# Optimization experiments

Hardware: AMD Instinct MI355X
Metric: run time of the kernel (lower is better)

The kernel has to match this reference:

```python
import jax, jax.numpy as jnp
import numpy as np

N, D, K = 20000, 128, 16   # nodes, distribution support size, padded neighbors (excl. self)
H = 2                      # number of barycenter hops (module's self.h)
EPS = 0.1                  # entropic regularization for the OT barycenter solver
SINK_ITERS = 20            # fixed Sinkhorn barycenter iterations
TINY = 1e-30


def setup_inputs() -> dict:
    key = jax.random.key(0)
    k1, k2, k3 = jax.random.split(key, 3)
    trans_X = jax.random.uniform(k1, (N, D), dtype=jnp.float32)
    costMatrix = jax.random.uniform(k2, (D, D), dtype=jnp.float32)
    neigh_idx = jax.random.randint(k3, (N, K), 0, N, dtype=jnp.int32)
    return {"trans_X": trans_X, "costMatrix": costMatrix, "neigh_idx": neigh_idx}


def _sinkhorn_barycenter(mu, Kmat, w):
    """Entropic Wasserstein barycenter (Benamou et al. iterative Bregman projections).
    mu:   [N, Kn, D] input distributions per node (rows sum to 1)
    Kmat: [D, D] Gibbs kernel exp(-C/eps)
    w:    [Kn] barycentric weights (sum to 1)
    returns b: [N, D] barycenter per node.
    """
    u0 = jnp.ones_like(mu)
    b0 = jnp.full(mu.shape[::2], 1.0 / mu.shape[-1], dtype=mu.dtype)  # [N, D]

    def step(carry, _):
        u, _b = carry
        # (K^T u): [N, Kn, D]
        KTu = jnp.einsum('ed,nke->nkd', Kmat, u) + TINY
        v = mu / KTu
        Kv = jnp.einsum('de,nke->nkd', Kmat, v) + TINY
        # geometric mean across the Kn input measures
        b = jnp.exp(jnp.einsum('k,nkd->nd', w, jnp.log(Kv)))
        u = b[:, None, :] / Kv
        return (u, b), None

    (_, b), _ = jax.lax.scan(step, (u0, b0), None, length=SINK_ITERS)
    return b


def reference(trans_X, costMatrix, neigh_idx):
    n = trans_X.shape[0]
    Kmat = jnp.exp(-costMatrix / EPS)  # [D, D]
    # append self node -> Kn = K + 1 members; uniform weights 1/degree (bary_weight='uniform')
    idx = jnp.concatenate([neigh_idx, jnp.arange(n, dtype=neigh_idx.dtype)[:, None]], axis=1)  # [N, Kn]
    Kn = idx.shape[1]
    w = jnp.full((Kn,), 1.0 / Kn, dtype=trans_X.dtype)

    X = trans_X
    for _ in range(H):
        mu = X[idx]                                    # gather neighbor dists [N, Kn, D]
        mu = mu / (jnp.sum(mu, axis=-1, keepdims=True) + TINY)
        X = _sinkhorn_barycenter(mu, Kmat, w)          # [N, D]
    return X
```

## Files before the change

### kernel.cpp

```cpp
#include <hip/hip_runtime.h>

#define D 128
#define NEIGH 16
#define SINKI 20
#define TINYF 1e-30f

typedef __attribute__((ext_vector_type(8))) _Float16 f16x8;
typedef __attribute__((ext_vector_type(2))) _Float16 f16x2;
typedef __attribute__((ext_vector_type(4))) float f32x4;
typedef __attribute__((ext_vector_type(2))) unsigned int u32x2;

template <int N>
__device__ __forceinline__ float rorf(float v) {
  int r = __builtin_amdgcn_update_dpp(0, __builtin_bit_cast(int, v),
                                      0x120 + N, 0xf, 0xf, true);
  return __builtin_bit_cast(float, r);
}

__device__ __forceinline__ f16x8 ldfrag(const _Float16* U, int k, int ks, int g) {
  return *(const f16x8*)((const char*)U + k * 256 + (((ks << 6) + (g << 4)) ^ ((k & 15) << 4)));
}

__device__ __forceinline__ void stquad(_Float16* U, int k, int rt, int g,
                                       float x, float y, float z, float w) {
  union { _Float16 h[4]; u32x2 u; } P;
  P.h[0] = (_Float16)x; P.h[1] = (_Float16)y;
  P.h[2] = (_Float16)z; P.h[3] = (_Float16)w;
  *(u32x2*)((char*)U + k * 256 + (((rt << 5) + (g << 3)) ^ ((k & 15) << 4))) = P.u;
}

__global__ __launch_bounds__(512, 1)
void wgcn_hop(const float* __restrict__ Xin,
              const float* __restrict__ Cmat,
              const int* __restrict__ neigh,
              float* __restrict__ Xout,
              int n_pairs) {
  __shared__ _Float16 KB[16384];
  __shared__ _Float16 KA[16384];
  __shared__ _Float16 US[8][4608];

  const int tid = threadIdx.x;

  for (int idx = tid; idx < 16384; idx += 512) {
    const int s = idx & 7, c = (idx >> 3) & 15, g = (idx >> 7) & 3;
    const int rt = (idx >> 9) & 7, ks = idx >> 12;
    const int e = (ks << 5) + (g << 3) + s;
    const int d = (rt << 4) + c;
    KB[idx] = (_Float16)(16.0f * expf(-10.0f * Cmat[e * 128 + d]));
    KA[idx] = (_Float16)(16.0f * expf(-10.0f * Cmat[d * 128 + e]));
  }
  __syncthreads();

  const int slot = tid >> 6;
  const int lane = tid & 63;
  const int g = lane >> 4;
  const int c = lane & 15;
  const int cc = (c < 2) ? c : 2;
  _Float16* U = US[slot];

  ((unsigned int*)U)[(34 << 6) | lane] = 0u;
  ((unsigned int*)U)[(35 << 6) | lane] = 0u;

  for (int p = blockIdx.x * 8 + slot; p < n_pairs; p += gridDim.x * 8) {
    const int nA = 2 * p, nB = 2 * p + 1;

    f32x4 mu0[8], mu1[8], muS[8], bvA[8], bvB[8];
    const int srcA = neigh[nA * NEIGH + c];
    const int srcB = neigh[nB * NEIGH + c];
    const int srcS = (c == 1) ? nB : nA;
#pragma unroll
    for (int rt = 0; rt < 8; ++rt) {
      mu0[rt] = *(const f32x4*)&Xin[(long)srcA * D + rt * 16 + g * 4];
      mu1[rt] = *(const f32x4*)&Xin[(long)srcB * D + rt * 16 + g * 4];
      muS[rt] = *(const f32x4*)&Xin[(long)srcS * D + rt * 16 + g * 4];
    }
    float s0 = 0.f, s1 = 0.f, sS = 0.f;
#pragma unroll
    for (int rt = 0; rt < 8; ++rt) {
      s0 += mu0[rt].x + mu0[rt].y + mu0[rt].z + mu0[rt].w;
      s1 += mu1[rt].x + mu1[rt].y + mu1[rt].z + mu1[rt].w;
      sS += muS[rt].x + muS[rt].y + muS[rt].z + muS[rt].w;
    }
    s0 += __shfl_xor(s0, 16, 64); s0 += __shfl_xor(s0, 32, 64);
    s1 += __shfl_xor(s1, 16, 64); s1 += __shfl_xor(s1, 32, 64);
    sS += __shfl_xor(sS, 16, 64); sS += __shfl_xor(sS, 32, 64);
    const float i0 = 1024.0f * __builtin_amdgcn_rcpf(s0 + TINYF);
    const float i1 = 1024.0f * __builtin_amdgcn_rcpf(s1 + TINYF);
    const float iS = 1024.0f * __builtin_amdgcn_rcpf(sS + TINYF);
#pragma unroll
    for (int rt = 0; rt < 8; ++rt) {
      mu0[rt].x *= i0; mu0[rt].y *= i0; mu0[rt].z *= i0; mu0[rt].w *= i0;
      mu1[rt].x *= i1; mu1[rt].y *= i1; mu1[rt].z *= i1; mu1[rt].w *= i1;
      muS[rt].x *= iS; muS[rt].y *= iS; muS[rt].z *= iS; muS[rt].w *= iS;
    }

#pragma unroll
    for (int j = 0; j < 34; ++j)
      ((unsigned int*)U)[(j << 6) | lane] = 0x3C003C00u;

    f16x8 pre1[4], pre2[4];
#pragma unroll
    for (int ks = 0; ks < 4; ++ks)
      pre1[ks] = *(const f16x8*)&KB[(((ks << 3) << 6) + lane) << 3];

    asm volatile("s_waitcnt lgkmcnt(0)" ::: "memory");

#pragma unroll 1
    for (int it = 0; it < SINKI; ++it) {
      f16x8 b0[4], b1[4], b2[4];
#pragma unroll
      for (int ks = 0; ks < 4; ++ks) {
        b0[ks] = ldfrag(U, c, ks, g);
        b1[ks] = ldfrag(U, 16 + c, ks, g);
        b2[ks] = ldfrag(U, 32 + cc, ks, g);
      }
#pragma unroll
      for (int rt = 0; rt < 8; ++rt) {
        f32x4 a0 = {0.f, 0.f, 0.f, 0.f}, a1 = a0, a2 = a0;
#pragma unroll
        for (int ks = 0; ks < 4; ++ks) {
          const f16x8 af = (rt == 0) ? pre1[ks]
              : *(const f16x8*)&KB[((((ks << 3) + rt) << 6) + lane) << 3];
          a0 = __builtin_amdgcn_mfma_f32_16x16x32_f16(af, b0[ks], a0, 0, 0, 0);
          a1 = __builtin_amdgcn_mfma_f32_16x16x32_f16(af, b1[ks], a1, 0, 0, 0);
          a2 = __builtin_amdgcn_mfma_f32_16x16x32_f16(af, b2[ks], a2, 0, 0, 0);
        }
        stquad(U, c, rt, g,
               mu0[rt].x * __builtin_amdgcn_rcpf(a0.x),
               mu0[rt].y * __builtin_amdgcn_rcpf(a0.y),
               mu0[rt].z * __builtin_amdgcn_rcpf(a0.z),
               mu0[rt].w * __builtin_amdgcn_rcpf(a0.w));
        stquad(U, 16 + c, rt, g,
               mu1[rt].x * __builtin_amdgcn_rcpf(a1.x),
               mu1[rt].y * __builtin_amdgcn_rcpf(a1.y),
               mu1[rt].z * __builtin_amdgcn_rcpf(a1.z),
               mu1[rt].w * __builtin_amdgcn_rcpf(a1.w));
        if (c < 2)
          stquad(U, 32 + c, rt, g,
                 muS[rt].x * __builtin_amdgcn_rcpf(a2.x),
                 muS[rt].y * __builtin_amdgcn_rcpf(a2.y),
                 muS[rt].z * __builtin_amdgcn_rcpf(a2.z),
                 muS[rt].w * __builtin_amdgcn_rcpf(a2.w));
      }
#pragma unroll
      for (int ks = 0; ks < 4; ++ks)
        pre2[ks] = *(const f16x8*)&KA[(((ks << 3) << 6) + lane) << 3];
      asm volatile("s_waitcnt lgkmcnt(0)" ::: "memory");

#pragma unroll
      for (int ks = 0; ks < 4; ++ks) {
        b0[ks] = ldfrag(U, c, ks, g);
        b1[ks] = ldfrag(U, 16 + c, ks, g);
        b2[ks] = ldfrag(U, 32 + cc, ks, g);
      }
#pragma unroll
      for (int rt = 0; rt < 8; ++rt) {
        f32x4 a0 = {0.f, 0.f, 0.f, 0.f}, a1 = a0, a2 = a0;
#pragma unroll
        for (int ks = 0; ks < 4; ++ks) {
          const f16x8 af = (rt == 0) ? pre2[ks]
              : *(const f16x8*)&KA[((((ks << 3) + rt) << 6) + lane) << 3];
          a0 = __builtin_amdgcn_mfma_f32_16x16x32_f16(af, b0[ks], a0, 0, 0, 0);
          a1 = __builtin_amdgcn_mfma_f32_16x16x32_f16(af, b1[ks], a1, 0, 0, 0);
          a2 = __builtin_amdgcn_mfma_f32_16x16x32_f16(af, b2[ks], a2, 0, 0, 0);
        }
        float bA[4], bB[4];
#pragma unroll
        for (int r = 0; r < 4; ++r) {
          const float tA = ((const float*)&a0)[r];
          const float tB = ((const float*)&a1)[r];
          const float tS = ((const float*)&a2)[r];
          float fA = (c == 0) ? tA * tS : tA;
          float fB = (c == 1) ? tB * tS : tB;
          float pA = __builtin_amdgcn_logf(fA);
          float pB = __builtin_amdgcn_logf(fB);
          pA += rorf<1>(pA); pA += rorf<2>(pA); pA += rorf<4>(pA); pA += rorf<8>(pA);
          pB += rorf<1>(pB); pB += rorf<2>(pB); pB += rorf<4>(pB); pB += rorf<8>(pB);
          bA[r] = __builtin_amdgcn_exp2f(pA * (1.0f / 17.0f));
          bB[r] = __builtin_amdgcn_exp2f(pB * (1.0f / 17.0f));
        }
        bvA[rt].x = bA[0]; bvA[rt].y = bA[1]; bvA[rt].z = bA[2]; bvA[rt].w = bA[3];
        bvB[rt].x = bB[0]; bvB[rt].y = bB[1]; bvB[rt].z = bB[2]; bvB[rt].w = bB[3];
        stquad(U, c, rt, g,
               bA[0] * __builtin_amdgcn_rcpf(((const float*)&a0)[0]),
               bA[1] * __builtin_amdgcn_rcpf(((const float*)&a0)[1]),
               bA[2] * __builtin_amdgcn_rcpf(((const float*)&a0)[2]),
               bA[3] * __builtin_amdgcn_rcpf(((const float*)&a0)[3]));
        stquad(U, 16 + c, rt, g,
               bB[0] * __builtin_amdgcn_rcpf(((const float*)&a1)[0]),
               bB[1] * __builtin_amdgcn_rcpf(((const float*)&a1)[1]),
               bB[2] * __builtin_amdgcn_rcpf(((const float*)&a1)[2]),
               bB[3] * __builtin_amdgcn_rcpf(((const float*)&a1)[3]));
        if (c < 2) {
          const float q0 = ((c == 0) ? bA[0] : bB[0]) * __builtin_amdgcn_rcpf(((const float*)&a2)[0]);
          const float q1 = ((c == 0) ? bA[1] : bB[1]) * __builtin_amdgcn_rcpf(((const float*)&a2)[1]);
          const float q2 = ((c == 0) ? bA[2] : bB[2]) * __builtin_amdgcn_rcpf(((const float*)&a2)[2]);
          const float q3 = ((c == 0) ? bA[3] : bB[3]) * __builtin_amdgcn_rcpf(((const float*)&a2)[3]);
          stquad(U, 32 + c, rt, g, q0, q1, q2, q3);
        }
      }
#pragma unroll
      for (int ks = 0; ks < 4; ++ks)
        pre1[ks] = *(const f16x8*)&KB[(((ks << 3) << 6) + lane) << 3];
      asm volatile("s_waitcnt lgkmcnt(0)" ::: "memory");
    }

    if (c < 2) {
      float* dst = &Xout[(long)((c == 0) ? nA : nB) * D];
#pragma unroll
      for (int rt = 0; rt < 8; ++rt) {
        const f32x4 bq = (c == 0) ? bvA[rt] : bvB[rt];
        f32x4 o;
        o.x = bq.x * (1.0f / 1024.0f);
        o.y = bq.y * (1.0f / 1024.0f);
        o.z = bq.z * (1.0f / 1024.0f);
        o.w = bq.w * (1.0f / 1024.0f);
        *(f32x4*)&dst[rt * 16 + g * 4] = o;
      }
    }
  }
}

extern "C" void kernel_launch(void* const* d_in, const int* in_sizes, int n_in,
                              void* d_out, int out_size, void* d_ws, size_t ws_size,
                              hipStream_t stream) {
  const float* trans_X = (const float*)d_in[0];
  const float* cost = (const float*)d_in[1];
  const int* neigh = (const int*)d_in[2];
  float* out = (float*)d_out;
  float* X1 = (float*)d_ws;
  const int n = in_sizes[0] / D;
  const int n_pairs = n / 2;

  dim3 grid(250), block(512);
  hipLaunchKernelGGL(wgcn_hop, grid, block, 0, stream, trans_X, cost, neigh, X1, n_pairs);
  hipLaunchKernelGGL(wgcn_hop, grid, block, 0, stream, X1, cost, neigh, out, n_pairs);
}
```

Baseline: 1.640 ms.

## Share self-node Sinkhorn matmuls across the block via shared-memory batching

In the old layout each wave ran a third MFMA stream for its two self-node columns, so most of that work was padding. The new layout packs the 16 self nodes of a block (2 per wave, 8 waves) into one shared 16-column tile. Each wave computes one row-tile of that shared product, and the results are exchanged through shared memory with block-wide barriers. This cuts the MFMA work per iteration by about a third and drops the last iteration's unused u update. The cost is three __syncthreads per Sinkhorn iteration, extra LDS traffic, and the h0/h1 accumulators held in registers until the barycenter step.

```diff
diff --git a/kernel.cpp b/kernel.cpp
--- a/kernel.cpp
+++ b/kernel.cpp
@@ -6,7 +6,6 @@
 #define TINYF 1e-30f
 
 typedef __attribute__((ext_vector_type(8))) _Float16 f16x8;
-typedef __attribute__((ext_vector_type(2))) _Float16 f16x2;
 typedef __attribute__((ext_vector_type(4))) float f32x4;
 typedef __attribute__((ext_vector_type(2))) unsigned int u32x2;
 
@@ -29,149 +28,177 @@
   *(u32x2*)((char*)U + k * 256 + (((rt << 5) + (g << 3)) ^ ((k & 15) << 4))) = P.u;
 }
 
+__device__ __forceinline__ int selfoff(int j, int rowbyte) {
+  return j * 512 + (rowbyte ^ (((j & 3) << 4) | ((j >> 2) << 6)));
+}
+
 __global__ __launch_bounds__(512, 1)
 void wgcn_hop(const float* __restrict__ Xin,
               const float* __restrict__ Cmat,
               const int* __restrict__ neigh,
               float* __restrict__ Xout,
-              int n_pairs) {
+              int n_batches) {
   __shared__ _Float16 KB[16384];
   __shared__ _Float16 KA[16384];
-  __shared__ _Float16 US[8][4608];
+  __shared__ _Float16 Us8[8][4096];
+  __shared__ _Float16 UselfU[2048];
+  __shared__ _Float16 UselfV[2048];
+  __shared__ float    MuSelf[2048];
+  __shared__ float    SelfKv[2048];
 
   const int tid = threadIdx.x;
 
   for (int idx = tid; idx < 16384; idx += 512) {
-    const int s = idx & 7, c = (idx >> 3) & 15, g = (idx >> 7) & 3;
-    const int rt = (idx >> 9) & 7, ks = idx >> 12;
-    const int e = (ks << 5) + (g << 3) + s;
-    const int d = (rt << 4) + c;
+    const int sI = idx & 7, cI = (idx >> 3) & 15, gI = (idx >> 7) & 3;
+    const int rtI = (idx >> 9) & 7, ksI = idx >> 12;
+    const int e = (ksI << 5) + (gI << 3) + sI;
+    const int d = (rtI << 4) + cI;
     KB[idx] = (_Float16)(16.0f * expf(-10.0f * Cmat[e * 128 + d]));
     KA[idx] = (_Float16)(16.0f * expf(-10.0f * Cmat[d * 128 + e]));
   }
-  __syncthreads();
 
   const int slot = tid >> 6;
   const int lane = tid & 63;
   const int g = lane >> 4;
   const int c = lane & 15;
-  const int cc = (c < 2) ? c : 2;
-  _Float16* U = US[slot];
-
-  ((unsigned int*)U)[(34 << 6) | lane] = 0u;
-  ((unsigned int*)U)[(35 << 6) | lane] = 0u;
-
-  for (int p = blockIdx.x * 8 + slot; p < n_pairs; p += gridDim.x * 8) {
-    const int nA = 2 * p, nB = 2 * p + 1;
-
-    f32x4 mu0[8], mu1[8], muS[8], bvA[8], bvB[8];
-    const int srcA = neigh[nA * NEIGH + c];
-    const int srcB = neigh[nB * NEIGH + c];
-    const int srcS = (c == 1) ? nB : nA;
-#pragma unroll
-    for (int rt = 0; rt < 8; ++rt) {
-      mu0[rt] = *(const f32x4*)&Xin[(long)srcA * D + rt * 16 + g * 4];
-      mu1[rt] = *(const f32x4*)&Xin[(long)srcB * D + rt * 16 + g * 4];
-      muS[rt] = *(const f32x4*)&Xin[(long)srcS * D + rt * 16 + g * 4];
+  _Float16* Us = Us8[slot];
+
+  for (int b = blockIdx.x; b < n_batches; b += gridDim.x) {
+    const int nA = b * 16 + 2 * slot, nB = nA + 1;
+
+    f32x4 mu0[8], mu1[8];
+    {
+      f32x4 muS[8];
+      const int srcA = neigh[nA * NEIGH + c];
+      const int srcB = neigh[nB * NEIGH + c];
+      const int srcS = (c == 1) ? nB : nA;
+      float s0 = 0.f, s1 = 0.f, sS = 0.f;
+#pragma unroll
+      for (int rt = 0; rt < 8; ++rt) {
+        mu0[rt] = *(const f32x4*)&Xin[(long)srcA * D + rt * 16 + g * 4];
+        mu1[rt] = *(const f32x4*)&Xin[(long)srcB * D + rt * 16 + g * 4];
+        muS[rt] = *(const f32x4*)&Xin[(long)srcS * D + rt * 16 + g * 4];
+        s0 += mu0[rt].x + mu0[rt].y + mu0[rt].z + mu0[rt].w;
+        s1 += mu1[rt].x + mu1[rt].y + mu1[rt].z + mu1[rt].w;
+        sS += muS[rt].x + muS[rt].y + muS[rt].z + muS[rt].w;
+      }
+      s0 += __shfl_xor(s0, 16, 64); s0 += __shfl_xor(s0, 32, 64);
+      s1 += __shfl_xor(s1, 16, 64); s1 += __shfl_xor(s1, 32, 64);
+      sS += __shfl_xor(sS, 16, 64); sS += __shfl_xor(sS, 32, 64);
+      const float i0 = 1024.0f * __builtin_amdgcn_rcpf(s0 + TINYF);
+      const float i1 = 1024.0f * __builtin_amdgcn_rcpf(s1 + TINYF);
+      const float iS = 1024.0f * __builtin_amdgcn_rcpf(sS + TINYF);
+#pragma unroll
+      for (int rt = 0; rt < 8; ++rt) {
+        mu0[rt].x *= i0; mu0[rt].y *= i0; mu0[rt].z *= i0; mu0[rt].w *= i0;
+        mu1[rt].x *= i1; mu1[rt].y *= i1; mu1[rt].z *= i1; mu1[rt].w *= i1;
+      }
+      if (c < 2) {
+        const int jme = 2 * slot + c;
+#pragma unroll
+        for (int rt = 0; rt < 8; ++rt) {
+          f32x4 m = muS[rt];
+          m.x *= iS; m.y *= iS; m.z *= iS; m.w *= iS;
+          *(f32x4*)((char*)MuSelf + selfoff(jme, (rt << 6) | (g << 4))) = m;
+        }
+      }
     }
-    float s0 = 0.f, s1 = 0.f, sS = 0.f;
-#pragma unroll
-    for (int rt = 0; rt < 8; ++rt) {
-      s0 += mu0[rt].x + mu0[rt].y + mu0[rt].z + mu0[rt].w;
-      s1 += mu1[rt].x + mu1[rt].y + mu1[rt].z + mu1[rt].w;
-      sS += muS[rt].x + muS[rt].y + muS[rt].z + muS[rt].w;
-    }
-    s0 += __shfl_xor(s0, 16, 64); s0 += __shfl_xor(s0, 32, 64);
-    s1 += __shfl_xor(s1, 16, 64); s1 += __shfl_xor(s1, 32, 64);
-    sS += __shfl_xor(sS, 16, 64); sS += __shfl_xor(sS, 32, 64);
-    const float i0 = 1024.0f * __builtin_amdgcn_rcpf(s0 + TINYF);
-    const float i1 = 1024.0f * __builtin_amdgcn_rcpf(s1 + TINYF);
-    const float iS = 1024.0f * __builtin_amdgcn_rcpf(sS + TINYF);
-#pragma unroll
-    for (int rt = 0; rt < 8; ++rt) {
-      mu0[rt].x *= i0; mu0[rt].y *= i0; mu0[rt].z *= i0; mu0[rt].w *= i0;
-      mu1[rt].x *= i1; mu1[rt].y *= i1; mu1[rt].z *= i1; mu1[rt].w *= i1;
-      muS[rt].x *= iS; muS[rt].y *= iS; muS[rt].z *= iS; muS[rt].w *= iS;
-    }
-
-#pragma unroll
-    for (int j = 0; j < 34; ++j)
-      ((unsigned int*)U)[(j << 6) | lane] = 0x3C003C00u;
-
-    f16x8 pre1[4], pre2[4];
-#pragma unroll
-    for (int ks = 0; ks < 4; ++ks)
-      pre1[ks] = *(const f16x8*)&KB[(((ks << 3) << 6) + lane) << 3];
-
-    asm volatile("s_waitcnt lgkmcnt(0)" ::: "memory");
+
+#pragma unroll
+    for (int j = 0; j < 32; ++j)
+      ((unsigned int*)Us)[(j << 6) | lane] = 0x3C003C00u;
+    ((unsigned int*)UselfU)[((2 * slot) << 6) | lane] = 0x3C003C00u;
+    ((unsigned int*)UselfU)[((2 * slot + 1) << 6) | lane] = 0x3C003C00u;
+    __syncthreads();
 
 #pragma unroll 1
     for (int it = 0; it < SINKI; ++it) {
       f16x8 b0[4], b1[4], b2[4];
 #pragma unroll
       for (int ks = 0; ks < 4; ++ks) {
-        b0[ks] = ldfrag(U, c, ks, g);
-        b1[ks] = ldfrag(U, 16 + c, ks, g);
-        b2[ks] = ldfrag(U, 32 + cc, ks, g);
-      }
-#pragma unroll
-      for (int rt = 0; rt < 8; ++rt) {
-        f32x4 a0 = {0.f, 0.f, 0.f, 0.f}, a1 = a0, a2 = a0;
-#pragma unroll
-        for (int ks = 0; ks < 4; ++ks) {
-          const f16x8 af = (rt == 0) ? pre1[ks]
-              : *(const f16x8*)&KB[((((ks << 3) + rt) << 6) + lane) << 3];
+        b0[ks] = ldfrag(Us, c, ks, g);
+        b1[ks] = ldfrag(Us, 16 + c, ks, g);
+        b2[ks] = ldfrag(UselfU, c, ks, g);
+      }
+      {
+        f32x4 a2 = {0.f, 0.f, 0.f, 0.f};
+#pragma unroll
+        for (int ks = 0; ks < 4; ++ks) {
+          const f16x8 af = *(const f16x8*)&KB[((((ks << 3) + slot) << 6) + lane) << 3];
+          a2 = __builtin_amdgcn_mfma_f32_16x16x32_f16(af, b2[ks], a2, 0, 0, 0);
+        }
+        const f32x4 ms = *(const f32x4*)((const char*)MuSelf + selfoff(c, (slot << 6) | (g << 4)));
+        stquad(UselfV, c, slot, g,
+               ms.x * __builtin_amdgcn_rcpf(a2.x),
+               ms.y * __builtin_amdgcn_rcpf(a2.y),
+               ms.z * __builtin_amdgcn_rcpf(a2.z),
+               ms.w * __builtin_amdgcn_rcpf(a2.w));
+      }
+#pragma unroll
+      for (int rt = 0; rt < 8; ++rt) {
+        f32x4 a0 = {0.f, 0.f, 0.f, 0.f}, a1 = a0;
+#pragma unroll
+        for (int ks = 0; ks < 4; ++ks) {
+          const f16x8 af = *(const f16x8*)&KB[((((ks << 3) + rt) << 6) + lane) << 3];
           a0 = __builtin_amdgcn_mfma_f32_16x16x32_f16(af, b0[ks], a0, 0, 0, 0);
           a1 = __builtin_amdgcn_mfma_f32_16x16x32_f16(af, b1[ks], a1, 0, 0, 0);
-          a2 = __builtin_amdgcn_mfma_f32_16x16x32_f16(af, b2[ks], a2, 0, 0, 0);
-        }
-        stquad(U, c, rt, g,
+        }
+        stquad(Us, c, rt, g,
                mu0[rt].x * __builtin_amdgcn_rcpf(a0.x),
                mu0[rt].y * __builtin_amdgcn_rcpf(a0.y),
                mu0[rt].z * __builtin_amdgcn_rcpf(a0.z),
                mu0[rt].w * __builtin_amdgcn_rcpf(a0.w));
-        stquad(U, 16 + c, rt, g,
+        stquad(Us, 16 + c, rt, g,
                mu1[rt].x * __builtin_amdgcn_rcpf(a1.x),
                mu1[rt].y * __builtin_amdgcn_rcpf(a1.y),
                mu1[rt].z * __builtin_amdgcn_rcpf(a1.z),
                mu1[rt].w * __builtin_amdgcn_rcpf(a1.w));
-        if (c < 2)
-          stquad(U, 32 + c, rt, g,
-                 muS[rt].x * __builtin_amdgcn_rcpf(a2.x),
-                 muS[rt].y * __builtin_amdgcn_rcpf(a2.y),
-                 muS[rt].z * __builtin_amdgcn_rcpf(a2.z),
-                 muS[rt].w * __builtin_amdgcn_rcpf(a2.w));
-      }
-#pragma unroll
-      for (int ks = 0; ks < 4; ++ks)
-        pre2[ks] = *(const f16x8*)&KA[(((ks << 3) << 6) + lane) << 3];
-      asm volatile("s_waitcnt lgkmcnt(0)" ::: "memory");
+      }
+      __syncthreads();
 
 #pragma unroll
       for (int ks = 0; ks < 4; ++ks) {
-        b0[ks] = ldfrag(U, c, ks, g);
-        b1[ks] = ldfrag(U, 16 + c, ks, g);
-        b2[ks] = ldfrag(U, 32 + cc, ks, g);
-      }
-#pragma unroll
-      for (int rt = 0; rt < 8; ++rt) {
-        f32x4 a0 = {0.f, 0.f, 0.f, 0.f}, a1 = a0, a2 = a0;
-#pragma unroll
-        for (int ks = 0; ks < 4; ++ks) {
-          const f16x8 af = (rt == 0) ? pre2[ks]
-              : *(const f16x8*)&KA[((((ks << 3) + rt) << 6) + lane) << 3];
+        b0[ks] = ldfrag(Us, c, ks, g);
+        b1[ks] = ldfrag(Us, 16 + c, ks, g);
+        b2[ks] = ldfrag(UselfV, c, ks, g);
+      }
+      {
+        f32x4 a2 = {0.f, 0.f, 0.f, 0.f};
+#pragma unroll
+        for (int ks = 0; ks < 4; ++ks) {
+          const f16x8 af = *(const f16x8*)&KA[((((ks << 3) + slot) << 6) + lane) << 3];
+          a2 = __builtin_amdgcn_mfma_f32_16x16x32_f16(af, b2[ks], a2, 0, 0, 0);
+        }
+        *(f32x4*)((char*)SelfKv + selfoff(c, (slot << 6) | (g << 4))) = a2;
+      }
+      f32x4 h0[8], h1[8];
+#pragma unroll
+      for (int rt = 0; rt < 8; ++rt) {
+        f32x4 a0 = {0.f, 0.f, 0.f, 0.f}, a1 = a0;
+#pragma unroll
+        for (int ks = 0; ks < 4; ++ks) {
+          const f16x8 af = *(const f16x8*)&KA[((((ks << 3) + rt) << 6) + lane) << 3];
           a0 = __builtin_amdgcn_mfma_f32_16x16x32_f16(af, b0[ks], a0, 0, 0, 0);
           a1 = __builtin_amdgcn_mfma_f32_16x16x32_f16(af, b1[ks], a1, 0, 0, 0);
-          a2 = __builtin_amdgcn_mfma_f32_16x16x32_f16(af, b2[ks], a2, 0, 0, 0);
-        }
+        }
+        h0[rt] = a0; h1[rt] = a1;
+      }
+      __syncthreads();
+
+      const int jme = 2 * slot + c;
+#pragma unroll
+      for (int rt = 0; rt < 8; ++rt) {
+        f32x4 sv = {1.f, 1.f, 1.f, 1.f};
+        if (c < 2)
+          sv = *(const f32x4*)((const char*)SelfKv + selfoff(jme, (rt << 6) | (g << 4)));
         float bA[4], bB[4];
 #pragma unroll
         for (int r = 0; r < 4; ++r) {
-          const float tA = ((const float*)&a0)[r];
-          const float tB = ((const float*)&a1)[r];
-          const float tS = ((const float*)&a2)[r];
-          float fA = (c == 0) ? tA * tS : tA;
-          float fB = (c == 1) ? tB * tS : tB;
+          const float tA = ((const float*)&h0[rt])[r];
+          const float tB = ((const float*)&h1[rt])[r];
+          const float svr = ((const float*)&sv)[r];
+          float fA = (c == 0) ? tA * svr : tA;
+          float fB = (c == 1) ? tB * svr : tB;
           float pA = __builtin_amdgcn_logf(fA);
           float pB = __builtin_amdgcn_logf(fB);
           pA += rorf<1>(pA); pA += rorf<2>(pA); pA += rorf<4>(pA); pA += rorf<8>(pA);
@@ -179,44 +206,35 @@
           bA[r] = __builtin_amdgcn_exp2f(pA * (1.0f / 17.0f));
           bB[r] = __builtin_amdgcn_exp2f(pB * (1.0f / 17.0f));
         }
-        bvA[rt].x = bA[0]; bvA[rt].y = bA[1]; bvA[rt].z = bA[2]; bvA[rt].w = bA[3];
-        bvB[rt].x = bB[0]; bvB[rt].y = bB[1]; bvB[rt].z = bB[2]; bvB[rt].w = bB[3];
-        stquad(U, c, rt, g,
-               bA[0] * __builtin_amdgcn_rcpf(((const float*)&a0)[0]),
-               bA[1] * __builtin_amdgcn_rcpf(((const float*)&a0)[1]),
-               bA[2] * __builtin_amdgcn_rcpf(((const float*)&a0)[2]),
-               bA[3] * __builtin_amdgcn_rcpf(((const float*)&a0)[3]));
-        stquad(U, 16 + c, rt, g,
-               bB[0] * __builtin_amdgcn_rcpf(((const float*)&a1)[0]),
-               bB[1] * __builtin_amdgcn_rcpf(((const float*)&a1)[1]),
-               bB[2] * __builtin_amdgcn_rcpf(((const float*)&a1)[2]),
-               bB[3] * __builtin_amdgcn_rcpf(((const float*)&a1)[3]));
-        if (c < 2) {
-          const float q0 = ((c == 0) ? bA[0] : bB[0]) * __builtin_amdgcn_rcpf(((const float*)&a2)[0]);
-          const float q1 = ((c == 0) ? bA[1] : bB[1]) * __builtin_amdgcn_rcpf(((const float*)&a2)[1]);
-          const float q2 = ((c == 0) ? bA[2] : bB[2]) * __builtin_amdgcn_rcpf(((const float*)&a2)[2]);
-          const float q3 = ((c == 0) ? bA[3] : bB[3]) * __builtin_amdgcn_rcpf(((const float*)&a2)[3]);
-          stquad(U, 32 + c, rt, g, q0, q1, q2, q3);
-        }
-      }
-#pragma unroll
-      for (int ks = 0; ks < 4; ++ks)
-        pre1[ks] = *(const f16x8*)&KB[(((ks << 3) << 6) + lane) << 3];
-      asm volatile("s_waitcnt lgkmcnt(0)" ::: "memory");
-    }
-
-    if (c < 2) {
-      float* dst = &Xout[(long)((c == 0) ? nA : nB) * D];
-#pragma unroll
-      for (int rt = 0; rt < 8; ++rt) {
-        const f32x4 bq = (c == 0) ? bvA[rt] : bvB[rt];
-        f32x4 o;
-        o.x = bq.x * (1.0f / 1024.0f);
-        o.y = bq.y * (1.0f / 1024.0f);
-        o.z = bq.z * (1.0f / 1024.0f);
-        o.w = bq.w * (1.0f / 1024.0f);
-        *(f32x4*)&dst[rt * 16 + g * 4] = o;
-      }
+        if (it < SINKI - 1) {
+          stquad(Us, c, rt, g,
+                 bA[0] * __builtin_amdgcn_rcpf(((const float*)&h0[rt])[0]),
+                 bA[1] * __builtin_amdgcn_rcpf(((const float*)&h0[rt])[1]),
+                 bA[2] * __builtin_amdgcn_rcpf(((const float*)&h0[rt])[2]),
+                 bA[3] * __builtin_amdgcn_rcpf(((const float*)&h0[rt])[3]));
+          stquad(Us, 16 + c, rt, g,
+                 bB[0] * __builtin_amdgcn_rcpf(((const float*)&h1[rt])[0]),
+                 bB[1] * __builtin_amdgcn_rcpf(((const float*)&h1[rt])[1]),
+                 bB[2] * __builtin_amdgcn_rcpf(((const float*)&h1[rt])[2]),
+                 bB[3] * __builtin_amdgcn_rcpf(((const float*)&h1[rt])[3]));
+          if (c < 2) {
+            const float q0 = ((c == 0) ? bA[0] : bB[0]) * __builtin_amdgcn_rcpf(((const float*)&sv)[0]);
+            const float q1 = ((c == 0) ? bA[1] : bB[1]) * __builtin_amdgcn_rcpf(((const float*)&sv)[1]);
+            const float q2 = ((c == 0) ? bA[2] : bB[2]) * __builtin_amdgcn_rcpf(((const float*)&sv)[2]);
+            const float q3 = ((c == 0) ? bA[3] : bB[3]) * __builtin_amdgcn_rcpf(((const float*)&sv)[3]);
+            stquad(UselfU, jme, rt, g, q0, q1, q2, q3);
+          }
+        } else if (c < 2) {
+          float* dst = &Xout[(long)((c == 0) ? nA : nB) * D + rt * 16 + g * 4];
+          f32x4 o;
+          o.x = ((c == 0) ? bA[0] : bB[0]) * (1.0f / 1024.0f);
+          o.y = ((c == 0) ? bA[1] : bB[1]) * (1.0f / 1024.0f);
+          o.z = ((c == 0) ? bA[2] : bB[2]) * (1.0f / 1024.0f);
+          o.w = ((c == 0) ? bA[3] : bB[3]) * (1.0f / 1024.0f);
+          *(f32x4*)dst = o;
+        }
+      }
+      __syncthreads();
     }
   }
 }
@@ -230,9 +248,9 @@
   float* out = (float*)d_out;
   float* X1 = (float*)d_ws;
   const int n = in_sizes[0] / D;
-  const int n_pairs = n / 2;
+  const int n_batches = n / 16;
 
   dim3 grid(250), block(512);
-  hipLaunchKernelGGL(wgcn_hop, grid, block, 0, stream, trans_X, cost, neigh, X1, n_pairs);
-  hipLaunchKernelGGL(wgcn_hop, grid, block, 0, stream, X1, cost, neigh, out, n_pairs);
-}
+  hipLaunchKernelGGL(wgcn_hop, grid, block, 0, stream, trans_X, cost, neigh, X1, n_batches);
+  hipLaunchKernelGGL(wgcn_hop, grid, block, 0, stream, X1, cost, neigh, out, n_batches);
+}
```

After: 1.656 ms. About the same (+1.0%).
